# Optimization experiments

Measured on AMD Instinct MI355X. Metric: run time of the kernel, lower is better.

## Reference

```python
import jax, jax.numpy as jnp
import numpy as np

L = 4      # number of layers (graph nodes)
B = 128    # batch
H = 4096   # neurons per layer


def setup_inputs() -> dict:
    key = jax.random.key(0)
    k1, k2, k3 = jax.random.split(key, 3)
    # per-layer source activations, stacked: [L, B, H]
    states = jax.random.normal(k1, (L, B, H), dtype=jnp.float32)
    # all Connection weight matrices, W[t, s] maps source s -> target t: [L, L, H_out, H_in]
    # scaled by 1/sqrt(H) so summed matmuls stay O(1) (original uses constant w_init)
    W = jax.random.normal(k2, (L, L, H, H), dtype=jnp.float32) * (1.0 / np.sqrt(H))
    # external inputs added into each target's current: [L, B, H]
    ext = jax.random.normal(k3, (L, B, H), dtype=jnp.float32)
    return {"states": states, "W": W, "ext": ext}


def reference(states, W, ext):
    # Synapses/Links: for each target t, sum over sources s of (x_s @ W[t,s].T)
    # (Connection.forward is x @ w.T). Single fused einsum replaces the
    # jit.fork fan-out over L*L small matmuls + Python-level sum.
    currents = jnp.einsum('sbh,tsoh->tbo', states, W) + ext  # [L, B, H]
    # Layer/Neurons: per-node activation function
    return jnp.tanh(currents)
```

## Files before the change

### kernel.cpp

```cpp
#include <hip/hip_runtime.h>
#include <hip/hip_bf16.h>
#include <stdint.h>

#define L_ 4
#define B_ 128
#define H_ 4096
#define BN 32
#define BKF 256
#define SUP 64
#define NTHR 256
#define NTOT (L_*B_*H_)
#define WTB (BN*BKF*2)

typedef _Float16 f16x8 __attribute__((ext_vector_type(8)));
typedef float    f32x4 __attribute__((ext_vector_type(4)));
typedef float    f4    __attribute__((ext_vector_type(4)));
typedef uint32_t u32x4 __attribute__((ext_vector_type(4)));
typedef uint32_t u32x2 __attribute__((ext_vector_type(2)));

__device__ __forceinline__ uint32_t pack2(float a, float b) {
  const _Float16 ha = (_Float16)a;
  const _Float16 hb = (_Float16)b;
  const uint32_t ua = (uint32_t)__builtin_bit_cast(uint16_t, ha);
  const uint32_t ub = (uint32_t)__builtin_bit_cast(uint16_t, hb);
  return ua | (ub << 16);
}

__global__ __launch_bounds__(NTHR)
void cvt_tile_kernel(const float* __restrict__ x, u32x4* __restrict__ ws)
{
  const int d   = blockIdx.x * NTHR + threadIdx.x;
  const int row = d & 127;
  const int lh  = (d >> 7) & 3;
  const int kk  = (d >> 9) & 1;
  const int kt  = d >> 10;
  const int s   = kt >> 6;
  const int kb  = kt & 63;
  const float* src = x + ((size_t)(s * B_ + row)) * H_ + kb * 64 + kk * 32 + lh * 8;
  f4 lo = *reinterpret_cast<const f4*>(src);
  f4 hi = *reinterpret_cast<const f4*>(src + 4);
  u32x4 v;
  v.x = pack2(lo.x, lo.y); v.y = pack2(lo.z, lo.w);
  v.z = pack2(hi.x, hi.y); v.w = pack2(hi.z, hi.w);
  ws[d] = v;
}

__device__ __forceinline__ void bar_lgkm0() {
  __builtin_amdgcn_sched_barrier(0);
  asm volatile("s_waitcnt lgkmcnt(0)");
  __builtin_amdgcn_sched_barrier(0);
  __builtin_amdgcn_s_barrier();
  __builtin_amdgcn_sched_barrier(0);
}

__global__ __launch_bounds__(NTHR, 2)
void net_gemm_kernel(const uint8_t* __restrict__ atiled,
                     const float* __restrict__ Wm,
                     const float* __restrict__ ext,
                     float* __restrict__ out)
{
  __shared__ __align__(16) uint8_t lds[2 * WTB];

  const int tid  = threadIdx.x;
  const int bid  = blockIdx.x;
  const int t    = bid >> 7;
  const int n0   = (bid & 127) * BN;

  const int wv   = tid >> 6;
  const int lane = tid & 63;
  const int lid  = lane & 15;
  const int lh   = lane >> 4;

  const uint8_t* a_base = atiled + lh * 2048 + (wv * 32 + lid) * 16;

  const float* wp0 = Wm + (((size_t)t * L_) * H_ + (size_t)(n0 + wv * 8)) * H_ + lane * 4;

  uint32_t b_rd[2][2];
  #pragma unroll
  for (int nf = 0; nf < 2; ++nf)
    #pragma unroll
    for (int kk = 0; kk < 2; ++kk) {
      const uint32_t row = (uint32_t)(nf * 16 + lid);
      b_rd[nf][kk] = row * 512 +
                     (((uint32_t)(kk * 64 + lh * 16)) ^ (((uint32_t)lid & 7) << 4));
    }

  f32x4 acc[2][2] = {};

  f4    wRA[8], wRB[8];
  f16x8 aA[2][2], aB[2][2];

  auto LOADW = [&](int j, f4 (&w)[8]) {
    const float* p = wp0 + (size_t)(j >> 4) * ((size_t)H_ * H_) + ((j & 15) << 8);
    #pragma unroll
    for (int i = 0; i < 8; ++i)
      w[i] = __builtin_nontemporal_load(reinterpret_cast<const f4*>(p + (size_t)i * H_));
  };

  auto WRITEW = [&](uint8_t* base, f4 (&w)[8]) {
    #pragma unroll
    for (int i = 0; i < 8; ++i) {
      u32x2 v;
      v.x = pack2(w[i].x, w[i].y);
      v.y = pack2(w[i].z, w[i].w);
      const uint32_t off = (uint32_t)wv * 4096 + (uint32_t)i * 512 +
                           (((uint32_t)lane * 8) ^ ((uint32_t)i << 4));
      *reinterpret_cast<u32x2*>(base + off) = v;
    }
  };

  auto LOADA = [&](int kt, f16x8 (&a)[2][2]) {
    const uint8_t* p = a_base + (size_t)kt * 16384;
    a[0][0] = *reinterpret_cast<const f16x8*>(p);
    a[1][0] = *reinterpret_cast<const f16x8*>(p + 256);
    a[0][1] = *reinterpret_cast<const f16x8*>(p + 8192);
    a[1][1] = *reinterpret_cast<const f16x8*>(p + 8192 + 256);
  };

  auto SUB = [&](const uint8_t* base, int skoff, f16x8 (&av)[2][2]) {
    f16x8 bv[2][2];
    #pragma unroll
    for (int nf = 0; nf < 2; ++nf)
      #pragma unroll
      for (int kk = 0; kk < 2; ++kk)
        bv[nf][kk] = *reinterpret_cast<const f16x8*>(base + b_rd[nf][kk] + skoff);
    #pragma unroll
    for (int kk = 0; kk < 2; ++kk)
      #pragma unroll
      for (int mf = 0; mf < 2; ++mf)
        #pragma unroll
        for (int nf = 0; nf < 2; ++nf)
          acc[mf][nf] = __builtin_amdgcn_mfma_f32_16x16x32_f16(
              av[mf][kk], bv[nf][kk], acc[mf][nf], 0, 0, 0);
  };

  uint8_t* buf0 = lds;
  uint8_t* buf1 = lds + WTB;

  LOADW(0, wRA);
  LOADW(1, wRB);
  LOADA(0, aA);
  WRITEW(buf0, wRA);
  bar_lgkm0();

  #define BODY(j_, WLD_, WWT_, BUFC_, BUFW_) do {  \
      LOADW((j_) + 2, WLD_);                       \
      LOADA(4*(j_) + 1, aB); SUB(BUFC_, 0,   aA);  \
      LOADA(4*(j_) + 2, aA); SUB(BUFC_, 128, aB);  \
      LOADA(4*(j_) + 3, aB); SUB(BUFC_, 256, aA);  \
      LOADA(4*(j_) + 4, aA); SUB(BUFC_, 384, aB);  \
      WRITEW(BUFW_, WWT_);                         \
      bar_lgkm0();                                 \
    } while (0)

  #pragma unroll 1
  for (int j = 0; j < 62; j += 2) {
    BODY(j,     wRA, wRB, buf0, buf1);
    BODY(j + 1, wRB, wRA, buf1, buf0);
  }
  LOADA(249, aB); SUB(buf0, 0,   aA);
  LOADA(250, aA); SUB(buf0, 128, aB);
  LOADA(251, aB); SUB(buf0, 256, aA);
  LOADA(252, aA); SUB(buf0, 384, aB);
  WRITEW(buf1, wRB);
  bar_lgkm0();
  LOADA(253, aB); SUB(buf1, 0,   aA);
  LOADA(254, aA); SUB(buf1, 128, aB);
  LOADA(255, aB); SUB(buf1, 256, aA);
                  SUB(buf1, 384, aB);
  #undef BODY

  #pragma unroll
  for (int mf = 0; mf < 2; ++mf)
    #pragma unroll
    for (int nf = 0; nf < 2; ++nf)
      #pragma unroll
      for (int j = 0; j < 4; ++j) {
        const int brow = wv * 32 + mf * 16 + lh * 4 + j;
        const int ocol = n0 + nf * 16 + lid;
        const size_t idx = ((size_t)(t * B_ + brow)) * H_ + ocol;
        out[idx] = tanhf(acc[mf][nf][j] + ext[idx]);
      }
}

#define FBK 64
#define FB_ABYTES (128*FBK*2)
#define FB_WBYTES (BN*FBK*2)
#define FB_BUFB   (FB_ABYTES+FB_WBYTES)
__global__ __launch_bounds__(NTHR, 2)
void net_gemm_fb(const float* __restrict__ statesf,
                 const float* __restrict__ Wm,
                 const float* __restrict__ ext,
                 float* __restrict__ out)
{
  __shared__ __align__(16) uint8_t lds[2 * FB_BUFB];

  const int tid  = threadIdx.x;
  const int bid  = blockIdx.x;
  const int t    = bid >> 7;
  const int n0   = (bid & 127) * BN;
  const int wv   = tid >> 6;
  const int lane = tid & 63;
  const int lid  = lane & 15;
  const int lh   = lane >> 4;

  const int arow = tid >> 3;
  const int acol = (tid & 7) * 8;
  const uint32_t a_st_off =
      (uint32_t)arow * 128 + (((uint32_t)(tid & 7) * 16) ^ ((uint32_t)(arow & 7) << 4));
  const float* af_base = statesf + (size_t)arow * H_ + acol;

  const int wrow = tid >> 4;
  const int wcol = (tid & 15) * 4;
  const float* w_base = Wm + ((size_t)t * L_ * H_ + (size_t)(n0 + wrow)) * H_ + wcol;
  const uint32_t w_st0 =
      (uint32_t)FB_ABYTES + (uint32_t)wrow * 128 + (((uint32_t)(tid & 15) * 8) ^ ((uint32_t)(wrow & 7) << 4));
  const uint32_t w_st1 = w_st0 + 16 * 128;

  uint32_t a_rd[2][2], b_rd[2][2];
  #pragma unroll
  for (int mf = 0; mf < 2; ++mf)
    #pragma unroll
    for (int kk = 0; kk < 2; ++kk) {
      const int row = wv * 32 + mf * 16 + lid;
      a_rd[mf][kk] = (uint32_t)row * 128 +
                     (((uint32_t)(kk * 64 + lh * 16)) ^ ((uint32_t)(lid & 7) << 4));
    }
  #pragma unroll
  for (int nf = 0; nf < 2; ++nf)
    #pragma unroll
    for (int kk = 0; kk < 2; ++kk) {
      const int row = nf * 16 + lid;
      b_rd[nf][kk] = (uint32_t)FB_ABYTES + (uint32_t)row * 128 +
                     (((uint32_t)(kk * 64 + lh * 16)) ^ ((uint32_t)(lid & 7) << 4));
    }

  f32x4 acc[2][2] = {};
  f4 af0[4][2], af1[4][2], wf0[2], wf1[2];

  auto LOADg = [&](int kidx, f4 (&af)[4][2], f4 (&wfx)[2]) {
    const int s  = kidx >> 6;
    const int h0 = (kidx & 63) << 6;
    const float* ap = af_base + (size_t)s * (B_ * H_) + h0;
    #pragma unroll
    for (int j = 0; j < 4; ++j) {
      af[j][0] = *reinterpret_cast<const f4*>(ap + (size_t)j * (32 * H_));
      af[j][1] = *reinterpret_cast<const f4*>(ap + (size_t)j * (32 * H_) + 4);
    }
    const float* wp = w_base + (size_t)s * ((size_t)H_ * H_) + h0;
    wfx[0] = __builtin_nontemporal_load(reinterpret_cast<const f4*>(wp));
    wfx[1] = __builtin_nontemporal_load(reinterpret_cast<const f4*>(wp + 16 * (size_t)H_));
  };

  auto WRITEg = [&](uint8_t* base, f4 (&af)[4][2], f4 (&wfx)[2]) {
    #pragma unroll
    for (int j = 0; j < 4; ++j) {
      u32x4 v;
      v.x = pack2(af[j][0].x, af[j][0].y);
      v.y = pack2(af[j][0].z, af[j][0].w);
      v.z = pack2(af[j][1].x, af[j][1].y);
      v.w = pack2(af[j][1].z, af[j][1].w);
      *reinterpret_cast<u32x4*>(base + j * 4096 + a_st_off) = v;
    }
    u32x2 w0, w1;
    w0.x = pack2(wfx[0].x, wfx[0].y); w0.y = pack2(wfx[0].z, wfx[0].w);
    w1.x = pack2(wfx[1].x, wfx[1].y); w1.y = pack2(wfx[1].z, wfx[1].w);
    *reinterpret_cast<u32x2*>(base + w_st0) = w0;
    *reinterpret_cast<u32x2*>(base + w_st1) = w1;
  };

  auto COMPUTE = [&](const uint8_t* base) {
    f16x8 av[2][2], bv[2][2];
    #pragma unroll
    for (int mf = 0; mf < 2; ++mf)
      #pragma unroll
      for (int kk = 0; kk < 2; ++kk)
        av[mf][kk] = *reinterpret_cast<const f16x8*>(base + a_rd[mf][kk]);
    #pragma unroll
    for (int nf = 0; nf < 2; ++nf)
      #pragma unroll
      for (int kk = 0; kk < 2; ++kk)
        bv[nf][kk] = *reinterpret_cast<const f16x8*>(base + b_rd[nf][kk]);
    #pragma unroll
    for (int kk = 0; kk < 2; ++kk)
      #pragma unroll
      for (int mf = 0; mf < 2; ++mf)
        #pragma unroll
        for (int nf = 0; nf < 2; ++nf)
          acc[mf][nf] = __builtin_amdgcn_mfma_f32_16x16x32_f16(
              av[mf][kk], bv[nf][kk], acc[mf][nf], 0, 0, 0);
  };

  uint8_t* buf0 = lds;
  uint8_t* buf1 = lds + FB_BUFB;

  LOADg(0, af0, wf0);
  LOADg(1, af1, wf1);
  WRITEg(buf0, af0, wf0);
  bar_lgkm0();

  #pragma unroll 1
  for (int k = 0; k < 256; k += 2) {
    if (k + 2 < 256) LOADg(k + 2, af0, wf0);
    COMPUTE(buf0);
    WRITEg(buf1, af1, wf1);
    bar_lgkm0();
    if (k + 3 < 256) LOADg(k + 3, af1, wf1);
    COMPUTE(buf1);
    if (k + 2 < 256) {
      WRITEg(buf0, af0, wf0);
      bar_lgkm0();
    }
  }

  #pragma unroll
  for (int mf = 0; mf < 2; ++mf)
    #pragma unroll
    for (int nf = 0; nf < 2; ++nf)
      #pragma unroll
      for (int j = 0; j < 4; ++j) {
        const int brow = wv * 32 + mf * 16 + lh * 4 + j;
        const int ocol = n0 + nf * 16 + lid;
        const size_t idx = ((size_t)(t * B_ + brow)) * H_ + ocol;
        out[idx] = tanhf(acc[mf][nf][j] + ext[idx]);
      }
}

extern "C" void kernel_launch(void* const* d_in, const int* in_sizes, int n_in,
                              void* d_out, int out_size, void* d_ws, size_t ws_size,
                              hipStream_t stream) {
  const float* states = (const float*)d_in[0];
  const float* W      = (const float*)d_in[1];
  const float* ext    = (const float*)d_in[2];
  float* out          = (float*)d_out;

  const size_t st_bytes = (size_t)NTOT * 2;
  if (ws_size >= st_bytes) {
    const int nunits = NTOT / 8;
    cvt_tile_kernel<<<nunits / NTHR, NTHR, 0, stream>>>(states, (u32x4*)d_ws);
    net_gemm_kernel<<<512, NTHR, 0, stream>>>(
        (const uint8_t*)d_ws, W, ext, out);
  } else {
    net_gemm_fb<<<512, NTHR, 0, stream>>>(states, W, ext, out);
  }
}
```

Measured before the change: 217.3 us.

## Double W K-tile to 512 and deepen A prefetch to two stages

Raises the per-stage K chunk of the weight tile from 256 to 512, so each lane loads 8 floats per row and writes 16-byte packed fp16 values into LDS. The number of barriers per K sweep halves. The weight global load is now issued after the barrier into a single register set rather than two alternating ones, and A fragments use a four-slot rotation so loads run two subtiles ahead of the MFMAs. LDS use doubles and register pressure rises, and the weight prefetch now covers only one stage, so memory latency may be less well hidden.

```diff
diff --git a/kernel.cpp b/kernel.cpp
--- a/kernel.cpp
+++ b/kernel.cpp
@@ -6,8 +6,8 @@
 #define B_ 128
 #define H_ 4096
 #define BN 32
-#define BKF 256
-#define SUP 64
+#define BKF 512
+#define SUP 32
 #define NTHR 256
 #define NTOT (L_*B_*H_)
 #define WTB (BN*BKF*2)
@@ -73,7 +73,7 @@
 
   const uint8_t* a_base = atiled + lh * 2048 + (wv * 32 + lid) * 16;
 
-  const float* wp0 = Wm + (((size_t)t * L_) * H_ + (size_t)(n0 + wv * 8)) * H_ + lane * 4;
+  const float* wp0 = Wm + (((size_t)t * L_) * H_ + (size_t)(n0 + wv * 8)) * H_ + (size_t)lane * 8;
 
   uint32_t b_rd[2][2];
   #pragma unroll
@@ -81,31 +81,35 @@
     #pragma unroll
     for (int kk = 0; kk < 2; ++kk) {
       const uint32_t row = (uint32_t)(nf * 16 + lid);
-      b_rd[nf][kk] = row * 512 +
+      b_rd[nf][kk] = row * 1024 +
                      (((uint32_t)(kk * 64 + lh * 16)) ^ (((uint32_t)lid & 7) << 4));
     }
 
   f32x4 acc[2][2] = {};
 
-  f4    wRA[8], wRB[8];
-  f16x8 aA[2][2], aB[2][2];
-
-  auto LOADW = [&](int j, f4 (&w)[8]) {
-    const float* p = wp0 + (size_t)(j >> 4) * ((size_t)H_ * H_) + ((j & 15) << 8);
-    #pragma unroll
-    for (int i = 0; i < 8; ++i)
-      w[i] = __builtin_nontemporal_load(reinterpret_cast<const f4*>(p + (size_t)i * H_));
-  };
-
-  auto WRITEW = [&](uint8_t* base, f4 (&w)[8]) {
+  f4    wR[16];
+  f16x8 aS0[2][2], aS1[2][2], aS2[2][2], aS3[2][2];
+
+  auto LOADW = [&](int j, f4 (&w)[16]) {
+    const float* p = wp0 + (size_t)(j >> 3) * ((size_t)H_ * H_) + ((j & 7) << 9);
     #pragma unroll
     for (int i = 0; i < 8; ++i) {
-      u32x2 v;
-      v.x = pack2(w[i].x, w[i].y);
-      v.y = pack2(w[i].z, w[i].w);
-      const uint32_t off = (uint32_t)wv * 4096 + (uint32_t)i * 512 +
-                           (((uint32_t)lane * 8) ^ ((uint32_t)i << 4));
-      *reinterpret_cast<u32x2*>(base + off) = v;
+      w[2*i]   = __builtin_nontemporal_load(reinterpret_cast<const f4*>(p + (size_t)i * H_));
+      w[2*i+1] = __builtin_nontemporal_load(reinterpret_cast<const f4*>(p + (size_t)i * H_ + 4));
+    }
+  };
+
+  auto WRITEW = [&](uint8_t* base, f4 (&w)[16]) {
+    #pragma unroll
+    for (int i = 0; i < 8; ++i) {
+      u32x4 v;
+      v.x = pack2(w[2*i].x,   w[2*i].y);
+      v.y = pack2(w[2*i].z,   w[2*i].w);
+      v.z = pack2(w[2*i+1].x, w[2*i+1].y);
+      v.w = pack2(w[2*i+1].z, w[2*i+1].w);
+      const uint32_t off = (uint32_t)(wv * 8 + i) * 1024 +
+                           (((uint32_t)lane * 16) ^ ((uint32_t)i << 4));
+      *reinterpret_cast<u32x4*>(base + off) = v;
     }
   };
 
@@ -137,38 +141,43 @@
   uint8_t* buf0 = lds;
   uint8_t* buf1 = lds + WTB;
 
-  LOADW(0, wRA);
-  LOADW(1, wRB);
-  LOADA(0, aA);
-  WRITEW(buf0, wRA);
+  LOADW(0, wR);
+  LOADA(0, aS0);
+  LOADA(1, aS1);
+  WRITEW(buf0, wR);
   bar_lgkm0();
-
-  #define BODY(j_, WLD_, WWT_, BUFC_, BUFW_) do {  \
-      LOADW((j_) + 2, WLD_);                       \
-      LOADA(4*(j_) + 1, aB); SUB(BUFC_, 0,   aA);  \
-      LOADA(4*(j_) + 2, aA); SUB(BUFC_, 128, aB);  \
-      LOADA(4*(j_) + 3, aB); SUB(BUFC_, 256, aA);  \
-      LOADA(4*(j_) + 4, aA); SUB(BUFC_, 384, aB);  \
-      WRITEW(BUFW_, WWT_);                         \
-      bar_lgkm0();                                 \
+  LOADW(1, wR);
+
+  #define ITER(j_, BC_, BW_, LW_) do {                    \
+      LOADA(8*(j_)+2, aS2); SUB(BC_, 0,   aS0);           \
+      LOADA(8*(j_)+3, aS3); SUB(BC_, 128, aS1);           \
+      LOADA(8*(j_)+4, aS0); SUB(BC_, 256, aS2);           \
+      LOADA(8*(j_)+5, aS1); SUB(BC_, 384, aS3);           \
+      LOADA(8*(j_)+6, aS2); SUB(BC_, 512, aS0);           \
+      LOADA(8*(j_)+7, aS3); SUB(BC_, 640, aS1);           \
+      LOADA(8*(j_)+8, aS0); SUB(BC_, 768, aS2);           \
+      LOADA(8*(j_)+9, aS1); SUB(BC_, 896, aS3);           \
+      WRITEW(BW_, wR);                                    \
+      bar_lgkm0();                                        \
+      if (LW_) LOADW((j_) + 2, wR);                       \
     } while (0)
 
   #pragma unroll 1
-  for (int j = 0; j < 62; j += 2) {
-    BODY(j,     wRA, wRB, buf0, buf1);
-    BODY(j + 1, wRB, wRA, buf1, buf0);
+  for (int jj = 0; jj < 30; jj += 2) {
+    ITER(jj,     buf0, buf1, 1);
+    ITER(jj + 1, buf1, buf0, 1);
   }
-  LOADA(249, aB); SUB(buf0, 0,   aA);
-  LOADA(250, aA); SUB(buf0, 128, aB);
-  LOADA(251, aB); SUB(buf0, 256, aA);
-  LOADA(252, aA); SUB(buf0, 384, aB);
-  WRITEW(buf1, wRB);
-  bar_lgkm0();
-  LOADA(253, aB); SUB(buf1, 0,   aA);
-  LOADA(254, aA); SUB(buf1, 128, aB);
-  LOADA(255, aB); SUB(buf1, 256, aA);
-                  SUB(buf1, 384, aB);
-  #undef BODY
+  ITER(30, buf0, buf1, 0);
+  #undef ITER
+
+  LOADA(250, aS2); SUB(buf1, 0,   aS0);
+  LOADA(251, aS3); SUB(buf1, 128, aS1);
+  LOADA(252, aS0); SUB(buf1, 256, aS2);
+  LOADA(253, aS1); SUB(buf1, 384, aS3);
+  LOADA(254, aS2); SUB(buf1, 512, aS0);
+  LOADA(255, aS3); SUB(buf1, 640, aS1);
+                   SUB(buf1, 768, aS2);
+                   SUB(buf1, 896, aS3);
 
   #pragma unroll
   for (int mf = 0; mf < 2; ++mf)
```

Measured after the change: 280.9 us. +29.3%, slower.

## Restructure main loop: single weight register buffer, batched A loads with sched barriers

Applied to the files above, without the earlier changes.

Replaces the two-deep register prefetch of weight tiles with a single register buffer loaded one stage ahead. The A-operand loads for a stage are now issued together up front and pinned with scheduling barriers. The goal is to cut register pressure and control instruction ordering so memory and MFMA work overlap better. In exchange, the global weight loads have less lead time before they are written to LDS, which may expose HBM latency.

```diff
diff --git a/kernel.cpp b/kernel.cpp
--- a/kernel.cpp
+++ b/kernel.cpp
@@ -7,7 +7,6 @@
 #define H_ 4096
 #define BN 32
 #define BKF 256
-#define SUP 64
 #define NTHR 256
 #define NTOT (L_*B_*H_)
 #define WTB (BN*BKF*2)
@@ -73,7 +72,7 @@
 
   const uint8_t* a_base = atiled + lh * 2048 + (wv * 32 + lid) * 16;
 
-  const float* wp0 = Wm + (((size_t)t * L_) * H_ + (size_t)(n0 + wv * 8)) * H_ + lane * 4;
+  const float* wp0 = Wm + (((size_t)t * L_) * H_ + (size_t)(n0 + wv * 8)) * H_ + (size_t)lane * 4;
 
   uint32_t b_rd[2][2];
   #pragma unroll
@@ -87,8 +86,8 @@
 
   f32x4 acc[2][2] = {};
 
-  f4    wRA[8], wRB[8];
-  f16x8 aA[2][2], aB[2][2];
+  f4    wR[8];
+  f16x8 aP[2][2], aQ[2][2], aR_[2][2], aS_[2][2];
 
   auto LOADW = [&](int j, f4 (&w)[8]) {
     const float* p = wp0 + (size_t)(j >> 4) * ((size_t)H_ * H_) + ((j & 15) << 8);
@@ -137,38 +136,42 @@
   uint8_t* buf0 = lds;
   uint8_t* buf1 = lds + WTB;
 
-  LOADW(0, wRA);
-  LOADW(1, wRB);
-  LOADA(0, aA);
-  WRITEW(buf0, wRA);
+  LOADW(0, wR);
+  LOADA(0, aP);
+  WRITEW(buf0, wR);
   bar_lgkm0();
 
-  #define BODY(j_, WLD_, WWT_, BUFC_, BUFW_) do {  \
-      LOADW((j_) + 2, WLD_);                       \
-      LOADA(4*(j_) + 1, aB); SUB(BUFC_, 0,   aA);  \
-      LOADA(4*(j_) + 2, aA); SUB(BUFC_, 128, aB);  \
-      LOADA(4*(j_) + 3, aB); SUB(BUFC_, 256, aA);  \
-      LOADA(4*(j_) + 4, aA); SUB(BUFC_, 384, aB);  \
-      WRITEW(BUFW_, WWT_);                         \
-      bar_lgkm0();                                 \
+  #define ITER(j_, BC_, BW_, LNEXT_) do {                 \
+      LOADA(4*(j_) + 1, aQ);                              \
+      LOADA(4*(j_) + 2, aR_);                             \
+      LOADA(4*(j_) + 3, aS_);                             \
+      __builtin_amdgcn_sched_barrier(0);                  \
+      LOADW((j_) + 1, wR);                                \
+      __builtin_amdgcn_sched_barrier(0);                  \
+      SUB(BC_, 0, aP);                                    \
+      if (LNEXT_) LOADA(4*(j_) + 4, aP);                  \
+      SUB(BC_, 128, aQ);                                  \
+      SUB(BC_, 256, aR_);                                 \
+      SUB(BC_, 384, aS_);                                 \
+      WRITEW(BW_, wR);                                    \
+      bar_lgkm0();                                        \
     } while (0)
 
   #pragma unroll 1
-  for (int j = 0; j < 62; j += 2) {
-    BODY(j,     wRA, wRB, buf0, buf1);
-    BODY(j + 1, wRB, wRA, buf1, buf0);
+  for (int jj = 0; jj < 62; jj += 2) {
+    ITER(jj,     buf0, buf1, 1);
+    ITER(jj + 1, buf1, buf0, 1);
   }
-  LOADA(249, aB); SUB(buf0, 0,   aA);
-  LOADA(250, aA); SUB(buf0, 128, aB);
-  LOADA(251, aB); SUB(buf0, 256, aA);
-  LOADA(252, aA); SUB(buf0, 384, aB);
-  WRITEW(buf1, wRB);
-  bar_lgkm0();
-  LOADA(253, aB); SUB(buf1, 0,   aA);
-  LOADA(254, aA); SUB(buf1, 128, aB);
-  LOADA(255, aB); SUB(buf1, 256, aA);
-                  SUB(buf1, 384, aB);
-  #undef BODY
+  ITER(62, buf0, buf1, 1);
+
+  LOADA(253, aQ);
+  LOADA(254, aR_);
+  LOADA(255, aS_);
+  SUB(buf1, 0,   aP);
+  SUB(buf1, 128, aQ);
+  SUB(buf1, 256, aR_);
+  SUB(buf1, 384, aS_);
+  #undef ITER
 
   #pragma unroll
   for (int mf = 0; mf < 2; ++mf)
```

After: 213.7 us. About the same (-1.6%).
